# Performance work log

Measured on AMD Instinct MI355X. Metric: run time of the kernel, lower is better.

Reference implementation:

```python
import jax, jax.numpy as jnp
import numpy as np
import math

D_MODEL = 1024
NUM_HEADS = 16
HEAD_DIM = D_MODEL // NUM_HEADS
REPETITIONS = 3
NEG = -10000.0


def setup_inputs() -> dict:
    key = jax.random.key(0)
    ks = jax.random.split(key, 5)
    B, S = 2, 2048
    x = jax.random.normal(ks[0], (B, S, D_MODEL), dtype=jnp.float32)
    Wqkv_w = jax.random.normal(ks[1], (3 * D_MODEL, D_MODEL), dtype=jnp.float32) * (1.0 / math.sqrt(D_MODEL))
    Wqkv_b = jax.random.normal(ks[2], (3 * D_MODEL,), dtype=jnp.float32) * 0.02
    out_w = jax.random.normal(ks[3], (D_MODEL, D_MODEL), dtype=jnp.float32) * (1.0 / math.sqrt(D_MODEL))
    out_b = jax.random.normal(ks[4], (D_MODEL,), dtype=jnp.float32) * 0.02
    return {"x": x, "Wqkv_w": Wqkv_w, "Wqkv_b": Wqkv_b, "out_w": out_w, "out_b": out_b}


def _self_attention(q, k, v, mask):
    # q,k,v: (B,S,H,D); mask: (S,S) additive causal (-10000 above diagonal)
    scale = 1.0 / math.sqrt(q.shape[-1])
    scores = jnp.einsum('bthd,bshd->bhts', q, k * scale) + mask  # (B,H,S,S)
    attn = jax.nn.softmax(scores, axis=-1)
    return jnp.einsum('bhts,bshd->bthd', attn, v)  # (B,S,H,D)


def reference(x, Wqkv_w, Wqkv_b, out_w, out_b):
    B, S, _ = x.shape
    qkv = x @ Wqkv_w.T + Wqkv_b                       # (B,S,3*D_MODEL)
    qkv = qkv.reshape(B, S, 3, NUM_HEADS, HEAD_DIM)
    q, k, v = qkv[:, :, 0], qkv[:, :, 1], qkv[:, :, 2]
    mask = jnp.triu(jnp.full((S, S), NEG, dtype=x.dtype), 1)
    context = _self_attention(q, k, v, mask)
    # recurrent re-attention: rep_dim == 'q' -> query replaced by previous context
    for _ in range(REPETITIONS - 1):
        context = _self_attention(context, k, v, mask)
    out = context.reshape(B, S, D_MODEL) @ out_w.T + out_b
    return out
```

## Files before the change

kernel.cpp:

```cpp
#include <hip/hip_runtime.h>


#define D_MODEL 1024
#define NHEADS  16
#define HD      64
#define SEQ     2048
#define BATCH   2
#define NROWS   (BATCH*SEQ)
#define NQKV    (3*D_MODEL)
#define SCL2F   0.1803368801111601f
#define MASK2   (-14426.950408889634f)

typedef __bf16 bf16x8 __attribute__((ext_vector_type(8)));
typedef float  f32x4  __attribute__((ext_vector_type(4)));
typedef unsigned short us8 __attribute__((ext_vector_type(8)));
typedef unsigned short us4 __attribute__((ext_vector_type(4)));
typedef short  s16x4  __attribute__((ext_vector_type(4)));

__device__ __forceinline__ unsigned short f2bf(float f) {
  unsigned int u = __float_as_uint(f);
  u = (u + 0x7fffu + ((u >> 16) & 1u)) >> 16;
  return (unsigned short)u;
}

union Pack8 { us8 v; unsigned short e[8]; };
union Pack4 { us4 v; unsigned short e[4]; };

__device__ __forceinline__ us8 cvt8(const float4 &a, const float4 &b) {
  Pack8 p;
  p.e[0]=f2bf(a.x); p.e[1]=f2bf(a.y); p.e[2]=f2bf(a.z); p.e[3]=f2bf(a.w);
  p.e[4]=f2bf(b.x); p.e[5]=f2bf(b.y); p.e[6]=f2bf(b.z); p.e[7]=f2bf(b.w);
  return p.v;
}

__device__ __forceinline__ void gl_lds16(const unsigned short* g, unsigned short* l) {
  __builtin_amdgcn_global_load_lds(
      (const __attribute__((address_space(1))) unsigned int*)g,
      (__attribute__((address_space(3))) unsigned int*)l, 16, 0, 0);
}

#define CVT_N1 (NROWS*D_MODEL)
#define CVT_N2 (NQKV*D_MODEL)
#define CVT_N3 (D_MODEL*D_MODEL)

__global__ __launch_bounds__(256) void cvt_all(
    const float* __restrict__ x, const float* __restrict__ wq,
    const float* __restrict__ ow,
    unsigned short* __restrict__ xb, unsigned short* __restrict__ wqb,
    unsigned short* __restrict__ owb)
{
  size_t i = ((size_t)blockIdx.x * 256 + threadIdx.x) * 8;
  const float* src; unsigned short* dst; size_t off;
  if (i < CVT_N1)                { src = x;  dst = xb;  off = i; }
  else if (i < CVT_N1 + CVT_N2)  { src = wq; dst = wqb; off = i - CVT_N1; }
  else                           { src = ow; dst = owb; off = i - CVT_N1 - CVT_N2; }
  float4 a = *(const float4*)(src + off);
  float4 b = *(const float4*)(src + off + 4);
  *(us8*)(dst + off) = cvt8(a, b);
}

__global__ __launch_bounds__(256) void qkv_gemm(
    const unsigned short* __restrict__ xb, const unsigned short* __restrict__ wqb,
    const float* __restrict__ bias,
    unsigned short* __restrict__ q, unsigned short* __restrict__ k,
    unsigned short* __restrict__ vT)
{
  __shared__ __align__(16) unsigned short smem[2*128*64];
  unsigned short* As = smem;
  unsigned short* Bs = smem + 128*64;
  const int tid = threadIdx.x;
  const int m0 = blockIdx.y * 128, n0 = blockIdx.x * 128;
  const int wave = tid >> 6, lane = tid & 63;
  const int wm = (wave >> 1) * 64, wn = (wave & 1) * 64;
  const int lrow = lane & 15, quad = lane >> 4;

  const int dr = lane >> 3;
  const int pg = lane & 7;
  const int sg = (pg ^ dr) * 8;
  const unsigned short* gA[4]; const unsigned short* gB[4];
  unsigned short *lA[4], *lB[4];
  #pragma unroll
  for (int i = 0; i < 4; i++) {
    int c = wave*4 + i;
    gA[i] = xb  + (size_t)(m0 + c*8 + dr) * D_MODEL + sg;
    gB[i] = wqb + (size_t)(n0 + c*8 + dr) * D_MODEL + sg;
    lA[i] = &As[c*512];
    lB[i] = &Bs[c*512];
  }
  const int px0 = (quad ^ (lrow & 7)) * 8;
  const int px1 = ((quad + 4) ^ (lrow & 7)) * 8;

  f32x4 acc[4][4];
  #pragma unroll
  for (int i = 0; i < 4; i++)
    #pragma unroll
    for (int j = 0; j < 4; j++) acc[i][j] = (f32x4){0.f,0.f,0.f,0.f};

  for (int k0 = 0; k0 < D_MODEL; k0 += 64) {
    __syncthreads();
    #pragma unroll
    for (int i = 0; i < 4; i++) { gl_lds16(gA[i] + k0, lA[i]); gl_lds16(gB[i] + k0, lB[i]); }
    __syncthreads();
    bf16x8 af[4][2], bfr[4][2];
    #pragma unroll
    for (int mf = 0; mf < 4; mf++) {
      int row = wm + mf*16 + lrow;
      af[mf][0] = *(const bf16x8*)&As[row*64 + px0];
      af[mf][1] = *(const bf16x8*)&As[row*64 + px1];
    }
    #pragma unroll
    for (int nb = 0; nb < 4; nb++) {
      int row = wn + nb*16 + lrow;
      bfr[nb][0] = *(const bf16x8*)&Bs[row*64 + px0];
      bfr[nb][1] = *(const bf16x8*)&Bs[row*64 + px1];
    }
    #pragma unroll
    for (int h = 0; h < 2; h++)
      #pragma unroll
      for (int mf = 0; mf < 4; mf++)
        #pragma unroll
        for (int nb = 0; nb < 4; nb++)
          acc[mf][nb] = __builtin_amdgcn_mfma_f32_16x16x32_bf16(af[mf][h], bfr[nb][h], acc[mf][nb], 0, 0, 0);
  }

  const int which = n0 >> 10;
  const int b  = m0 >> 11;
  const int s0 = m0 & 2047;
  const int h0 = (n0 & 1023) >> 6;

  __syncthreads();

  if (which < 2) {
    const float scl = (which == 0) ? SCL2F : 1.0f;
    #pragma unroll
    for (int nb = 0; nb < 4; nb++) {
      int n = wn + nb*16 + lrow;
      float bi = bias[n0 + n];
      #pragma unroll
      for (int mf = 0; mf < 4; mf++) {
        int m = wm + mf*16 + quad*4;
        #pragma unroll
        for (int r = 0; r < 4; r++)
          smem[(m + r)*128 + n] = f2bf((acc[mf][nb][r] + bi) * scl);
      }
    }
    __syncthreads();
    unsigned short* dstbase = (which == 0) ? q : k;
    const int hh   = wave >> 1;
    const int half = wave & 1;
    unsigned short* hb = dstbase + ((size_t)((b*NHEADS + h0 + hh)*SEQ + s0))*HD;
    #pragma unroll
    for (int i = 0; i < 8; i++) {
      int off  = half*4096 + i*512 + lane*8;
      int s    = off >> 6;
      int slot = off & 63;
      *(uint4*)(hb + off) = *(const uint4*)&smem[s*128 + hh*64 + slot];
    }
  } else {
    #pragma unroll
    for (int nb = 0; nb < 4; nb++) {
      int n = wn + nb*16 + lrow;
      float bi = bias[n0 + n];
      int sw = (n & 7) << 3;
      #pragma unroll
      for (int mf = 0; mf < 4; mf++) {
        int m = wm + mf*16 + quad*4;
        Pack4 p4;
        #pragma unroll
        for (int r = 0; r < 4; r++) p4.e[r] = f2bf(acc[mf][nb][r] + bi);
        *(us4*)&smem[n*128 + (m ^ sw)] = p4.v;
      }
    }
    __syncthreads();
    #pragma unroll
    for (int i = 0; i < 8; i++) {
      int n  = wave*32 + i*4 + (lane >> 4);
      int mo = (lane & 15) * 8;
      int sw = (n & 7) << 3;
      unsigned short* dst = vT +
          ((size_t)((b*NHEADS + h0 + (n >> 6))*HD + (n & 63)))*SEQ + s0 + mo;
      *(uint4*)dst = *(const uint4*)&smem[n*128 + (mo ^ sw)];
    }
  }
}

#define LDQ 72

__global__ __launch_bounds__(512, 4) void attn3(
    const unsigned short* __restrict__ qg,
    const unsigned short* __restrict__ kg,
    const unsigned short* __restrict__ vTg,
    unsigned short* __restrict__ ctx)
{
  __shared__ __align__(16) unsigned short Ks[4][64*LDQ];
  __shared__ __align__(16) unsigned short Vs[4][64*LDQ];
  unsigned short* QC = &Vs[0][0];

  const int tid  = threadIdx.x;
  const int w    = tid >> 6, lane = tid & 63;
  const int lrow = lane & 15, quad = lane >> 4;
  const int bh = blockIdx.x;
  const int yy = blockIdx.y;
  const int base = (blockIdx.x + yy) & 7;
  const int qt = (yy < 8) ? base : (15 - base);
  const unsigned short* qbase = qg  + (size_t)bh * SEQ * HD;
  const unsigned short* kbase = kg  + (size_t)bh * SEQ * HD;
  const unsigned short* vbase = vTg + (size_t)bh * HD * SEQ;
  unsigned short* cbase = ctx + (size_t)bh * SEQ * HD;

  const int srow = tid >> 3;
  const int sco  = (tid & 7) * 8;
  const int qrow = tid >> 2, qc0 = (tid & 3) * 16;
  const bool vsw = (w & 1);
  const int vq = (quad*4) ^ ((lrow >> 3) << 2);

  {
    const unsigned short* src = qbase + (size_t)(qt*128 + qrow)*HD + qc0;
    *(uint4*)&QC[qrow*LDQ + qc0]     = *(const uint4*)src;
    *(uint4*)&QC[qrow*LDQ + qc0 + 8] = *(const uint4*)(src + 8);
  }
  __syncthreads();

  bf16x8 qb0 = *(const bf16x8*)&QC[(w*16 + lrow)*LDQ + quad*8];
  bf16x8 qb1 = *(const bf16x8*)&QC[(w*16 + lrow)*LDQ + 32 + quad*8];
  __syncthreads();

  const int qwbase = qt*128 + w*16;
  const int npair = qt + 1;

  for (int rep = 0; rep < 3; ++rep) {
    f32x4 od[4];
    #pragma unroll
    for (int df = 0; df < 4; df++) od[df] = (f32x4){0.f,0.f,0.f,0.f};
    float ls = 0.f;

    uint4 ka, kb, va, vb;
    {
      const unsigned short* ks = kbase + (size_t)srow*HD + sco;
      ka = *(const uint4*)ks;  kb = *(const uint4*)(ks + 64*HD);
      const unsigned short* vs = vbase + (size_t)srow*SEQ + sco;
      va = *(const uint4*)vs;  vb = *(const uint4*)(vs + 64);
    }

    for (int t = 0; t < npair; ++t) {
      const int pb = (t & 1) * 2;
      *(uint4*)&Ks[pb][srow*LDQ + sco]   = ka;
      *(uint4*)&Ks[pb+1][srow*LDQ + sco] = kb;
      {
        uint4 vaS = vsw ? make_uint4(va.z, va.w, va.x, va.y) : va;
        uint4 vbS = vsw ? make_uint4(vb.z, vb.w, vb.x, vb.y) : vb;
        *(uint4*)&Vs[pb][srow*LDQ + sco]   = vaS;
        *(uint4*)&Vs[pb+1][srow*LDQ + sco] = vbS;
      }
      if (t + 1 < npair) {
        const unsigned short* ks = kbase + (size_t)((2*t+2)*64 + srow)*HD + sco;
        ka = *(const uint4*)ks;  kb = *(const uint4*)(ks + 64*HD);
        const unsigned short* vs = vbase + (size_t)srow*SEQ + (2*t+2)*64 + sco;
        va = *(const uint4*)vs;  vb = *(const uint4*)(vs + 64);
      }
      __syncthreads();

      #pragma unroll
      for (int half = 0; half < 2; ++half) {
        const int bb = pb + half;
        const int sbase = (2*t + half) * 64;
        if (sbase > qwbase + 15) continue;
        f32x4 sc[4];
        __builtin_amdgcn_s_setprio(1);
        #pragma unroll
        for (int sf = 0; sf < 4; sf++) {
          bf16x8 a0 = *(const bf16x8*)&Ks[bb][(sf*16 + lrow)*LDQ + quad*8];
          bf16x8 a1 = *(const bf16x8*)&Ks[bb][(sf*16 + lrow)*LDQ + 32 + quad*8];
          f32x4 z = (f32x4){0.f,0.f,0.f,0.f};
          z = __builtin_amdgcn_mfma_f32_16x16x32_bf16(a0, qb0, z, 0, 0, 0);
          z = __builtin_amdgcn_mfma_f32_16x16x32_bf16(a1, qb1, z, 0, 0, 0);
          sc[sf] = z;
        }
        __builtin_amdgcn_s_setprio(0);
        if (sbase + 63 > qwbase) {
          int ql = qwbase + lrow;
          #pragma unroll
          for (int sf = 0; sf < 4; sf++)
            #pragma unroll
            for (int r = 0; r < 4; r++)
              if (sbase + sf*16 + quad*4 + r > ql) sc[sf][r] += MASK2;
        }
        s16x4 pf[4];
        float lp = 0.f;
        #pragma unroll
        for (int sf = 0; sf < 4; sf++) {
          Pack4 pk;
          #pragma unroll
          for (int r = 0; r < 4; r++) {
            float pe = __builtin_amdgcn_exp2f(sc[sf][r]);
            lp += pe;
            pk.e[r] = __builtin_bit_cast(unsigned short, (__bf16)pe);
          }
          pf[sf] = __builtin_bit_cast(s16x4, pk.v);
        }
        ls += lp;
        __builtin_amdgcn_s_setprio(1);
        #pragma unroll
        for (int df = 0; df < 4; df++) {
          s16x4 v0 = *(const s16x4*)&Vs[bb][(df*16 + lrow)*LDQ +  0 + vq];
          s16x4 v1 = *(const s16x4*)&Vs[bb][(df*16 + lrow)*LDQ + 16 + vq];
          s16x4 v2 = *(const s16x4*)&Vs[bb][(df*16 + lrow)*LDQ + 32 + vq];
          s16x4 v3 = *(const s16x4*)&Vs[bb][(df*16 + lrow)*LDQ + 48 + vq];
          od[df] = __builtin_amdgcn_mfma_f32_16x16x16bf16_1k(v0, pf[0], od[df], 0, 0, 0);
          od[df] = __builtin_amdgcn_mfma_f32_16x16x16bf16_1k(v1, pf[1], od[df], 0, 0, 0);
          od[df] = __builtin_amdgcn_mfma_f32_16x16x16bf16_1k(v2, pf[2], od[df], 0, 0, 0);
          od[df] = __builtin_amdgcn_mfma_f32_16x16x16bf16_1k(v3, pf[3], od[df], 0, 0, 0);
        }
        __builtin_amdgcn_s_setprio(0);
      }
    }

    ls += __shfl_xor(ls, 16);
    ls += __shfl_xor(ls, 32);

    __syncthreads();
    {
      float f = ((rep < 2) ? SCL2F : 1.0f) / ls;
      #pragma unroll
      for (int df = 0; df < 4; df++) {
        Pack4 pk;
        #pragma unroll
        for (int r = 0; r < 4; r++)
          pk.e[r] = __builtin_bit_cast(unsigned short, (__bf16)(od[df][r] * f));
        *(us4*)&QC[(w*16 + lrow)*LDQ + df*16 + quad*4] = pk.v;
      }
    }
    __syncthreads();
    if (rep < 2) {
      qb0 = *(const bf16x8*)&QC[(w*16 + lrow)*LDQ + quad*8];
      qb1 = *(const bf16x8*)&QC[(w*16 + lrow)*LDQ + 32 + quad*8];
      __syncthreads();
    }
  }

  {
    unsigned short* dst = cbase + (size_t)(qt*128 + qrow)*HD + qc0;
    *(uint4*)dst       = *(const uint4*)&QC[qrow*LDQ + qc0];
    *(uint4*)(dst + 8) = *(const uint4*)&QC[qrow*LDQ + qc0 + 8];
  }
}

__global__ __launch_bounds__(256) void out_gemm(
    const unsigned short* __restrict__ ctx, const unsigned short* __restrict__ owb,
    const float* __restrict__ bias, float* __restrict__ out)
{
  __shared__ __align__(16) unsigned short As[128*64];
  __shared__ __align__(16) unsigned short Bs[64*64];
  const int tid = threadIdx.x;
  const int m0 = blockIdx.y * 128, n0 = blockIdx.x * 64;
  const int wave = tid >> 6, lane = tid & 63;
  const int wm = (wave >> 1) * 64, wn = (wave & 1) * 32;
  const int lrow = lane & 15, quad = lane >> 4;

  const int dr = lane >> 3, pg = lane & 7;
  const int sg = (pg ^ dr) * 8;
  size_t aoff[4]; unsigned short* lA[4];
  #pragma unroll
  for (int i = 0; i < 4; i++) {
    int c = wave*4 + i;
    int row = m0 + c*8 + dr;
    aoff[i] = ((size_t)((row >> 11)*NHEADS)*SEQ + (row & 2047))*HD + sg;
    lA[i] = &As[c*512];
  }
  const unsigned short* gB[2]; unsigned short* lB[2];
  #pragma unroll
  for (int j = 0; j < 2; j++) {
    int c = wave*2 + j;
    gB[j] = owb + (size_t)(n0 + c*8 + dr) * D_MODEL + sg;
    lB[j] = &Bs[c*512];
  }
  const int px0 = (quad ^ (lrow & 7)) * 8;
  const int px1 = ((quad + 4) ^ (lrow & 7)) * 8;

  f32x4 acc[4][2];
  #pragma unroll
  for (int i = 0; i < 4; i++)
    #pragma unroll
    for (int j = 0; j < 2; j++) acc[i][j] = (f32x4){0.f,0.f,0.f,0.f};

  for (int k0 = 0; k0 < D_MODEL; k0 += 64) {
    size_t hoff = (size_t)(k0 >> 6) * SEQ * HD;
    __syncthreads();
    #pragma unroll
    for (int i = 0; i < 4; i++) gl_lds16(ctx + aoff[i] + hoff, lA[i]);
    #pragma unroll
    for (int j = 0; j < 2; j++) gl_lds16(gB[j] + k0, lB[j]);
    __syncthreads();
    bf16x8 af[4][2], bfr[2][2];
    #pragma unroll
    for (int mf = 0; mf < 4; mf++) {
      int row = wm + mf*16 + lrow;
      af[mf][0] = *(const bf16x8*)&As[row*64 + px0];
      af[mf][1] = *(const bf16x8*)&As[row*64 + px1];
    }
    #pragma unroll
    for (int nb = 0; nb < 2; nb++) {
      int row = wn + nb*16 + lrow;
      bfr[nb][0] = *(const bf16x8*)&Bs[row*64 + px0];
      bfr[nb][1] = *(const bf16x8*)&Bs[row*64 + px1];
    }
    #pragma unroll
    for (int h = 0; h < 2; h++)
      #pragma unroll
      for (int mf = 0; mf < 4; mf++)
        #pragma unroll
        for (int nb = 0; nb < 2; nb++)
          acc[mf][nb] = __builtin_amdgcn_mfma_f32_16x16x32_bf16(af[mf][h], bfr[nb][h], acc[mf][nb], 0, 0, 0);
  }

  #pragma unroll
  for (int mf = 0; mf < 4; mf++) {
    #pragma unroll
    for (int nb = 0; nb < 2; nb++) {
      #pragma unroll
      for (int r = 0; r < 4; r++) {
        int mm = m0 + wm + mf*16 + quad*4 + r;
        int n  = n0 + wn + nb*16 + lrow;
        out[(size_t)mm * D_MODEL + n] = acc[mf][nb][r] + bias[n];
      }
    }
  }
}

extern "C" void kernel_launch(void* const* d_in, const int* in_sizes, int n_in,
                              void* d_out, int out_size, void* d_ws, size_t ws_size,
                              hipStream_t stream) {
  (void)in_sizes; (void)n_in; (void)out_size; (void)ws_size;
  const float* x      = (const float*)d_in[0];
  const float* Wqkv_w = (const float*)d_in[1];
  const float* Wqkv_b = (const float*)d_in[2];
  const float* out_w  = (const float*)d_in[3];
  const float* out_b  = (const float*)d_in[4];
  float* out = (float*)d_out;

  unsigned short* ws = (unsigned short*)d_ws;
  unsigned short* xb  = ws;
  unsigned short* wqb = ws + CVT_N1;
  unsigned short* owb = ws + CVT_N1 + CVT_N2;
  unsigned short* q   = ws + CVT_N1 + CVT_N2 + CVT_N3;
  unsigned short* k   = q + (size_t)NROWS*D_MODEL;
  unsigned short* vT  = k + (size_t)NROWS*D_MODEL;
  unsigned short* ctx = xb;

  cvt_all<<<(CVT_N1+CVT_N2+CVT_N3)/(256*8), 256, 0, stream>>>(x, Wqkv_w, out_w, xb, wqb, owb);
  qkv_gemm<<<dim3(NQKV/128, NROWS/128), 256, 0, stream>>>(xb, wqb, Wqkv_b, q, k, vT);
  attn3<<<dim3(BATCH*NHEADS, SEQ/128), 512, 0, stream>>>(q, k, vT, ctx);
  out_gemm<<<dim3(D_MODEL/64, NROWS/128), 256, 0, stream>>>(ctx, owb, out_b, out);
}
```

Measured before the change: 219.2 us.

## Shrink attention query tile to 64 rows with 256-thread blocks

The attention kernel now processes 64 query rows per block with 4 waves instead of 128 rows with 8 waves. The grid doubles to 32 query tiles per head, and each iteration consumes a single 64-key tile instead of a pair. Shared buffers shrink to two stages, and a new four-group tile ordering is meant to balance the causal workload across blocks. This gives more, smaller blocks and less masked-out work per block at the diagonal, but each K/V tile is now reused by fewer queries and there are more barriers per unit of work.

```diff
diff --git a/kernel.cpp b/kernel.cpp
--- a/kernel.cpp
+++ b/kernel.cpp
@@ -186,14 +186,14 @@
 
 #define LDQ 72
 
-__global__ __launch_bounds__(512, 4) void attn3(
+__global__ __launch_bounds__(256, 4) void attn3(
     const unsigned short* __restrict__ qg,
     const unsigned short* __restrict__ kg,
     const unsigned short* __restrict__ vTg,
     unsigned short* __restrict__ ctx)
 {
-  __shared__ __align__(16) unsigned short Ks[4][64*LDQ];
-  __shared__ __align__(16) unsigned short Vs[4][64*LDQ];
+  __shared__ __align__(16) unsigned short Ks[2][64*LDQ];
+  __shared__ __align__(16) unsigned short Vs[2][64*LDQ];
   unsigned short* QC = &Vs[0][0];
 
   const int tid  = threadIdx.x;
@@ -201,23 +201,24 @@
   const int lrow = lane & 15, quad = lane >> 4;
   const int bh = blockIdx.x;
   const int yy = blockIdx.y;
-  const int base = (blockIdx.x + yy) & 7;
-  const int qt = (yy < 8) ? base : (15 - base);
+  const int sgrp = yy >> 3, g = yy & 7;
+  const int e = (bh + g) & 7;
+  const int qt = (sgrp == 0) ? e : (sgrp == 1) ? (31 - e)
+               : (sgrp == 2) ? (15 - e) : (16 + e);
   const unsigned short* qbase = qg  + (size_t)bh * SEQ * HD;
   const unsigned short* kbase = kg  + (size_t)bh * SEQ * HD;
   const unsigned short* vbase = vTg + (size_t)bh * HD * SEQ;
   unsigned short* cbase = ctx + (size_t)bh * SEQ * HD;
 
-  const int srow = tid >> 3;
-  const int sco  = (tid & 7) * 8;
-  const int qrow = tid >> 2, qc0 = (tid & 3) * 16;
-  const bool vsw = (w & 1);
+  const int srow = tid >> 2;
+  const int sco  = (tid & 3) * 16;
+  const bool vsw = (srow >> 3) & 1;
   const int vq = (quad*4) ^ ((lrow >> 3) << 2);
 
   {
-    const unsigned short* src = qbase + (size_t)(qt*128 + qrow)*HD + qc0;
-    *(uint4*)&QC[qrow*LDQ + qc0]     = *(const uint4*)src;
-    *(uint4*)&QC[qrow*LDQ + qc0 + 8] = *(const uint4*)(src + 8);
+    const unsigned short* src = qbase + (size_t)(qt*64 + srow)*HD + sco;
+    *(uint4*)&QC[srow*LDQ + sco]     = *(const uint4*)src;
+    *(uint4*)&QC[srow*LDQ + sco + 8] = *(const uint4*)(src + 8);
   }
   __syncthreads();
 
@@ -225,8 +226,8 @@
   bf16x8 qb1 = *(const bf16x8*)&QC[(w*16 + lrow)*LDQ + 32 + quad*8];
   __syncthreads();
 
-  const int qwbase = qt*128 + w*16;
-  const int npair = qt + 1;
+  const int qwbase = qt*64 + w*16;
+  const int nt = qt + 1;
 
   for (int rep = 0; rep < 3; ++rep) {
     f32x4 od[4];
@@ -234,85 +235,80 @@
     for (int df = 0; df < 4; df++) od[df] = (f32x4){0.f,0.f,0.f,0.f};
     float ls = 0.f;
 
-    uint4 ka, kb, va, vb;
+    uint4 ka0, ka1, va0, va1;
     {
       const unsigned short* ks = kbase + (size_t)srow*HD + sco;
-      ka = *(const uint4*)ks;  kb = *(const uint4*)(ks + 64*HD);
+      ka0 = *(const uint4*)ks;  ka1 = *(const uint4*)(ks + 8);
       const unsigned short* vs = vbase + (size_t)srow*SEQ + sco;
-      va = *(const uint4*)vs;  vb = *(const uint4*)(vs + 64);
-    }
-
-    for (int t = 0; t < npair; ++t) {
-      const int pb = (t & 1) * 2;
-      *(uint4*)&Ks[pb][srow*LDQ + sco]   = ka;
-      *(uint4*)&Ks[pb+1][srow*LDQ + sco] = kb;
+      va0 = *(const uint4*)vs;  va1 = *(const uint4*)(vs + 8);
+    }
+
+    for (int t = 0; t < nt; ++t) {
+      const int bb = t & 1;
+      *(uint4*)&Ks[bb][srow*LDQ + sco]     = ka0;
+      *(uint4*)&Ks[bb][srow*LDQ + sco + 8] = ka1;
       {
-        uint4 vaS = vsw ? make_uint4(va.z, va.w, va.x, va.y) : va;
-        uint4 vbS = vsw ? make_uint4(vb.z, vb.w, vb.x, vb.y) : vb;
-        *(uint4*)&Vs[pb][srow*LDQ + sco]   = vaS;
-        *(uint4*)&Vs[pb+1][srow*LDQ + sco] = vbS;
-      }
-      if (t + 1 < npair) {
-        const unsigned short* ks = kbase + (size_t)((2*t+2)*64 + srow)*HD + sco;
-        ka = *(const uint4*)ks;  kb = *(const uint4*)(ks + 64*HD);
-        const unsigned short* vs = vbase + (size_t)srow*SEQ + (2*t+2)*64 + sco;
-        va = *(const uint4*)vs;  vb = *(const uint4*)(vs + 64);
+        uint4 vaS = vsw ? make_uint4(va0.z, va0.w, va0.x, va0.y) : va0;
+        uint4 vbS = vsw ? make_uint4(va1.z, va1.w, va1.x, va1.y) : va1;
+        *(uint4*)&Vs[bb][srow*LDQ + sco]     = vaS;
+        *(uint4*)&Vs[bb][srow*LDQ + sco + 8] = vbS;
+      }
+      if (t + 1 < nt) {
+        const unsigned short* ks = kbase + (size_t)((t+1)*64 + srow)*HD + sco;
+        ka0 = *(const uint4*)ks;  ka1 = *(const uint4*)(ks + 8);
+        const unsigned short* vs = vbase + (size_t)srow*SEQ + (t+1)*64 + sco;
+        va0 = *(const uint4*)vs;  va1 = *(const uint4*)(vs + 8);
       }
       __syncthreads();
 
-      #pragma unroll
-      for (int half = 0; half < 2; ++half) {
-        const int bb = pb + half;
-        const int sbase = (2*t + half) * 64;
-        if (sbase > qwbase + 15) continue;
-        f32x4 sc[4];
-        __builtin_amdgcn_s_setprio(1);
-        #pragma unroll
-        for (int sf = 0; sf < 4; sf++) {
-          bf16x8 a0 = *(const bf16x8*)&Ks[bb][(sf*16 + lrow)*LDQ + quad*8];
-          bf16x8 a1 = *(const bf16x8*)&Ks[bb][(sf*16 + lrow)*LDQ + 32 + quad*8];
-          f32x4 z = (f32x4){0.f,0.f,0.f,0.f};
-          z = __builtin_amdgcn_mfma_f32_16x16x32_bf16(a0, qb0, z, 0, 0, 0);
-          z = __builtin_amdgcn_mfma_f32_16x16x32_bf16(a1, qb1, z, 0, 0, 0);
-          sc[sf] = z;
+      const int sbase = t * 64;
+      f32x4 sc[4];
+      __builtin_amdgcn_s_setprio(1);
+      #pragma unroll
+      for (int sf = 0; sf < 4; sf++) {
+        bf16x8 a0 = *(const bf16x8*)&Ks[bb][(sf*16 + lrow)*LDQ + quad*8];
+        bf16x8 a1 = *(const bf16x8*)&Ks[bb][(sf*16 + lrow)*LDQ + 32 + quad*8];
+        f32x4 z = (f32x4){0.f,0.f,0.f,0.f};
+        z = __builtin_amdgcn_mfma_f32_16x16x32_bf16(a0, qb0, z, 0, 0, 0);
+        z = __builtin_amdgcn_mfma_f32_16x16x32_bf16(a1, qb1, z, 0, 0, 0);
+        sc[sf] = z;
+      }
+      __builtin_amdgcn_s_setprio(0);
+      if (sbase + 63 > qwbase) {
+        int ql = qwbase + lrow;
+        #pragma unroll
+        for (int sf = 0; sf < 4; sf++)
+          #pragma unroll
+          for (int r = 0; r < 4; r++)
+            if (sbase + sf*16 + quad*4 + r > ql) sc[sf][r] += MASK2;
+      }
+      s16x4 pf[4];
+      float lp = 0.f;
+      #pragma unroll
+      for (int sf = 0; sf < 4; sf++) {
+        Pack4 pk;
+        #pragma unroll
+        for (int r = 0; r < 4; r++) {
+          float pe = __builtin_amdgcn_exp2f(sc[sf][r]);
+          lp += pe;
+          pk.e[r] = __builtin_bit_cast(unsigned short, (__bf16)pe);
         }
-        __builtin_amdgcn_s_setprio(0);
-        if (sbase + 63 > qwbase) {
-          int ql = qwbase + lrow;
-          #pragma unroll
-          for (int sf = 0; sf < 4; sf++)
-            #pragma unroll
-            for (int r = 0; r < 4; r++)
-              if (sbase + sf*16 + quad*4 + r > ql) sc[sf][r] += MASK2;
-        }
-        s16x4 pf[4];
-        float lp = 0.f;
-        #pragma unroll
-        for (int sf = 0; sf < 4; sf++) {
-          Pack4 pk;
-          #pragma unroll
-          for (int r = 0; r < 4; r++) {
-            float pe = __builtin_amdgcn_exp2f(sc[sf][r]);
-            lp += pe;
-            pk.e[r] = __builtin_bit_cast(unsigned short, (__bf16)pe);
-          }
-          pf[sf] = __builtin_bit_cast(s16x4, pk.v);
-        }
-        ls += lp;
-        __builtin_amdgcn_s_setprio(1);
-        #pragma unroll
-        for (int df = 0; df < 4; df++) {
-          s16x4 v0 = *(const s16x4*)&Vs[bb][(df*16 + lrow)*LDQ +  0 + vq];
-          s16x4 v1 = *(const s16x4*)&Vs[bb][(df*16 + lrow)*LDQ + 16 + vq];
-          s16x4 v2 = *(const s16x4*)&Vs[bb][(df*16 + lrow)*LDQ + 32 + vq];
-          s16x4 v3 = *(const s16x4*)&Vs[bb][(df*16 + lrow)*LDQ + 48 + vq];
-          od[df] = __builtin_amdgcn_mfma_f32_16x16x16bf16_1k(v0, pf[0], od[df], 0, 0, 0);
-          od[df] = __builtin_amdgcn_mfma_f32_16x16x16bf16_1k(v1, pf[1], od[df], 0, 0, 0);
-          od[df] = __builtin_amdgcn_mfma_f32_16x16x16bf16_1k(v2, pf[2], od[df], 0, 0, 0);
-          od[df] = __builtin_amdgcn_mfma_f32_16x16x16bf16_1k(v3, pf[3], od[df], 0, 0, 0);
-        }
-        __builtin_amdgcn_s_setprio(0);
-      }
+        pf[sf] = __builtin_bit_cast(s16x4, pk.v);
+      }
+      ls += lp;
+      __builtin_amdgcn_s_setprio(1);
+      #pragma unroll
+      for (int df = 0; df < 4; df++) {
+        s16x4 v0 = *(const s16x4*)&Vs[bb][(df*16 + lrow)*LDQ +  0 + vq];
+        s16x4 v1 = *(const s16x4*)&Vs[bb][(df*16 + lrow)*LDQ + 16 + vq];
+        s16x4 v2 = *(const s16x4*)&Vs[bb][(df*16 + lrow)*LDQ + 32 + vq];
+        s16x4 v3 = *(const s16x4*)&Vs[bb][(df*16 + lrow)*LDQ + 48 + vq];
+        od[df] = __builtin_amdgcn_mfma_f32_16x16x16bf16_1k(v0, pf[0], od[df], 0, 0, 0);
+        od[df] = __builtin_amdgcn_mfma_f32_16x16x16bf16_1k(v1, pf[1], od[df], 0, 0, 0);
+        od[df] = __builtin_amdgcn_mfma_f32_16x16x16bf16_1k(v2, pf[2], od[df], 0, 0, 0);
+        od[df] = __builtin_amdgcn_mfma_f32_16x16x16bf16_1k(v3, pf[3], od[df], 0, 0, 0);
+      }
+      __builtin_amdgcn_s_setprio(0);
     }
 
     ls += __shfl_xor(ls, 16);
@@ -339,9 +335,9 @@
   }
 
   {
-    unsigned short* dst = cbase + (size_t)(qt*128 + qrow)*HD + qc0;
-    *(uint4*)dst       = *(const uint4*)&QC[qrow*LDQ + qc0];
-    *(uint4*)(dst + 8) = *(const uint4*)&QC[qrow*LDQ + qc0 + 8];
+    unsigned short* dst = cbase + (size_t)(qt*64 + srow)*HD + sco;
+    *(uint4*)dst       = *(const uint4*)&QC[srow*LDQ + sco];
+    *(uint4*)(dst + 8) = *(const uint4*)&QC[srow*LDQ + sco + 8];
   }
 }
 
@@ -449,6 +445,6 @@
 
   cvt_all<<<(CVT_N1+CVT_N2+CVT_N3)/(256*8), 256, 0, stream>>>(x, Wqkv_w, out_w, xb, wqb, owb);
   qkv_gemm<<<dim3(NQKV/128, NROWS/128), 256, 0, stream>>>(xb, wqb, Wqkv_b, q, k, vT);
-  attn3<<<dim3(BATCH*NHEADS, SEQ/128), 512, 0, stream>>>(q, k, vT, ctx);
+  attn3<<<dim3(BATCH*NHEADS, 32), 256, 0, stream>>>(q, k, vT, ctx);
   out_gemm<<<dim3(D_MODEL/64, NROWS/128), 256, 0, stream>>>(ctx, owb, out_b, out);
 }
```

Measured after the change: 220.6 us. No clear change (+0.6%).

## Load attention K/V tiles directly into LDS with XOR-swizzled layout

Applied to the files above, without the earlier changes.

Replaces the register-staged K/V prefetch (global load to VGPR, then ds_write) in the attention kernel with direct global-to-LDS loads via gl_lds16, double-buffered across tile pairs. The padded LDQ=72 layout becomes an unpadded 64-wide layout with an XOR swizzle to avoid bank conflicts, and all Q/K/V/context LDS addressing is updated to match. This is meant to cut VGPR pressure and ds_write instructions and reduce LDS footprint. The trade-off is that synchronisation moves to the end of each tile iteration, so correctness depends on the async LDS writes being complete at that barrier.

```diff
diff --git a/kernel.cpp b/kernel.cpp
--- a/kernel.cpp
+++ b/kernel.cpp
@@ -184,16 +184,14 @@
   }
 }
 
-#define LDQ 72
-
 __global__ __launch_bounds__(512, 4) void attn3(
     const unsigned short* __restrict__ qg,
     const unsigned short* __restrict__ kg,
     const unsigned short* __restrict__ vTg,
     unsigned short* __restrict__ ctx)
 {
-  __shared__ __align__(16) unsigned short Ks[4][64*LDQ];
-  __shared__ __align__(16) unsigned short Vs[4][64*LDQ];
+  __shared__ __align__(16) unsigned short Ks[4][64*64];
+  __shared__ __align__(16) unsigned short Vs[4][64*64];
   unsigned short* QC = &Vs[0][0];
 
   const int tid  = threadIdx.x;
@@ -209,20 +207,31 @@
   unsigned short* cbase = ctx + (size_t)bh * SEQ * HD;
 
   const int srow = tid >> 3;
-  const int sco  = (tid & 7) * 8;
-  const int qrow = tid >> 2, qc0 = (tid & 3) * 16;
-  const bool vsw = (w & 1);
-  const int vq = (quad*4) ^ ((lrow >> 3) << 2);
-
+  const int su   = (((tid & 7) ^ (srow & 7)) * 8);
+  unsigned short* const wdst_k[4] = { &Ks[0][(tid>>6)*512], &Ks[1][(tid>>6)*512],
+                                      &Ks[2][(tid>>6)*512], &Ks[3][(tid>>6)*512] };
+  unsigned short* const wdst_v[4] = { &Vs[0][(tid>>6)*512], &Vs[1][(tid>>6)*512],
+                                      &Vs[2][(tid>>6)*512], &Vs[3][(tid>>6)*512] };
+
+  const int kx0 = (quad ^ (lrow & 7)) * 8;
+  const int kx1 = ((quad + 4) ^ (lrow & 7)) * 8;
+  int vx[4];
+  #pragma unroll
+  for (int c = 0; c < 4; c++)
+    vx[c] = (((2*c + (quad >> 1)) ^ (lrow & 7)) * 8) + (quad & 1) * 4;
+
+  const int qrow = tid >> 2, qj = tid & 3;
+  const int qu0 = ((2*qj)     ^ (qrow & 7)) * 8;
+  const int qu1 = ((2*qj + 1) ^ (qrow & 7)) * 8;
   {
-    const unsigned short* src = qbase + (size_t)(qt*128 + qrow)*HD + qc0;
-    *(uint4*)&QC[qrow*LDQ + qc0]     = *(const uint4*)src;
-    *(uint4*)&QC[qrow*LDQ + qc0 + 8] = *(const uint4*)(src + 8);
+    const unsigned short* src = qbase + (size_t)(qt*128 + qrow)*HD + qj*16;
+    *(uint4*)&QC[qrow*64 + qu0] = *(const uint4*)src;
+    *(uint4*)&QC[qrow*64 + qu1] = *(const uint4*)(src + 8);
   }
   __syncthreads();
 
-  bf16x8 qb0 = *(const bf16x8*)&QC[(w*16 + lrow)*LDQ + quad*8];
-  bf16x8 qb1 = *(const bf16x8*)&QC[(w*16 + lrow)*LDQ + 32 + quad*8];
+  bf16x8 qb0 = *(const bf16x8*)&QC[(w*16 + lrow)*64 + kx0];
+  bf16x8 qb1 = *(const bf16x8*)&QC[(w*16 + lrow)*64 + kx1];
   __syncthreads();
 
   const int qwbase = qt*128 + w*16;
@@ -234,31 +243,21 @@
     for (int df = 0; df < 4; df++) od[df] = (f32x4){0.f,0.f,0.f,0.f};
     float ls = 0.f;
 
-    uint4 ka, kb, va, vb;
-    {
-      const unsigned short* ks = kbase + (size_t)srow*HD + sco;
-      ka = *(const uint4*)ks;  kb = *(const uint4*)(ks + 64*HD);
-      const unsigned short* vs = vbase + (size_t)srow*SEQ + sco;
-      va = *(const uint4*)vs;  vb = *(const uint4*)(vs + 64);
-    }
+    gl_lds16(kbase + (size_t)srow*HD + su,        wdst_k[0]);
+    gl_lds16(kbase + (size_t)(64 + srow)*HD + su, wdst_k[1]);
+    gl_lds16(vbase + (size_t)srow*SEQ + su,       wdst_v[0]);
+    gl_lds16(vbase + (size_t)srow*SEQ + 64 + su,  wdst_v[1]);
+    __syncthreads();
 
     for (int t = 0; t < npair; ++t) {
       const int pb = (t & 1) * 2;
-      *(uint4*)&Ks[pb][srow*LDQ + sco]   = ka;
-      *(uint4*)&Ks[pb+1][srow*LDQ + sco] = kb;
-      {
-        uint4 vaS = vsw ? make_uint4(va.z, va.w, va.x, va.y) : va;
-        uint4 vbS = vsw ? make_uint4(vb.z, vb.w, vb.x, vb.y) : vb;
-        *(uint4*)&Vs[pb][srow*LDQ + sco]   = vaS;
-        *(uint4*)&Vs[pb+1][srow*LDQ + sco] = vbS;
-      }
       if (t + 1 < npair) {
-        const unsigned short* ks = kbase + (size_t)((2*t+2)*64 + srow)*HD + sco;
-        ka = *(const uint4*)ks;  kb = *(const uint4*)(ks + 64*HD);
-        const unsigned short* vs = vbase + (size_t)srow*SEQ + (2*t+2)*64 + sco;
-        va = *(const uint4*)vs;  vb = *(const uint4*)(vs + 64);
-      }
-      __syncthreads();
+        const int npb = pb ^ 2;
+        gl_lds16(kbase + (size_t)((2*t+2)*64 + srow)*HD + su, wdst_k[npb]);
+        gl_lds16(kbase + (size_t)((2*t+3)*64 + srow)*HD + su, wdst_k[npb+1]);
+        gl_lds16(vbase + (size_t)srow*SEQ + (2*t+2)*64 + su,  wdst_v[npb]);
+        gl_lds16(vbase + (size_t)srow*SEQ + (2*t+3)*64 + su,  wdst_v[npb+1]);
+      }
 
       #pragma unroll
       for (int half = 0; half < 2; ++half) {
@@ -269,8 +268,8 @@
         __builtin_amdgcn_s_setprio(1);
         #pragma unroll
         for (int sf = 0; sf < 4; sf++) {
-          bf16x8 a0 = *(const bf16x8*)&Ks[bb][(sf*16 + lrow)*LDQ + quad*8];
-          bf16x8 a1 = *(const bf16x8*)&Ks[bb][(sf*16 + lrow)*LDQ + 32 + quad*8];
+          bf16x8 a0 = *(const bf16x8*)&Ks[bb][(sf*16 + lrow)*64 + kx0];
+          bf16x8 a1 = *(const bf16x8*)&Ks[bb][(sf*16 + lrow)*64 + kx1];
           f32x4 z = (f32x4){0.f,0.f,0.f,0.f};
           z = __builtin_amdgcn_mfma_f32_16x16x32_bf16(a0, qb0, z, 0, 0, 0);
           z = __builtin_amdgcn_mfma_f32_16x16x32_bf16(a1, qb1, z, 0, 0, 0);
@@ -302,10 +301,10 @@
         __builtin_amdgcn_s_setprio(1);
         #pragma unroll
         for (int df = 0; df < 4; df++) {
-          s16x4 v0 = *(const s16x4*)&Vs[bb][(df*16 + lrow)*LDQ +  0 + vq];
-          s16x4 v1 = *(const s16x4*)&Vs[bb][(df*16 + lrow)*LDQ + 16 + vq];
-          s16x4 v2 = *(const s16x4*)&Vs[bb][(df*16 + lrow)*LDQ + 32 + vq];
-          s16x4 v3 = *(const s16x4*)&Vs[bb][(df*16 + lrow)*LDQ + 48 + vq];
+          s16x4 v0 = *(const s16x4*)&Vs[bb][(df*16 + lrow)*64 + vx[0]];
+          s16x4 v1 = *(const s16x4*)&Vs[bb][(df*16 + lrow)*64 + vx[1]];
+          s16x4 v2 = *(const s16x4*)&Vs[bb][(df*16 + lrow)*64 + vx[2]];
+          s16x4 v3 = *(const s16x4*)&Vs[bb][(df*16 + lrow)*64 + vx[3]];
           od[df] = __builtin_amdgcn_mfma_f32_16x16x16bf16_1k(v0, pf[0], od[df], 0, 0, 0);
           od[df] = __builtin_amdgcn_mfma_f32_16x16x16bf16_1k(v1, pf[1], od[df], 0, 0, 0);
           od[df] = __builtin_amdgcn_mfma_f32_16x16x16bf16_1k(v2, pf[2], od[df], 0, 0, 0);
@@ -313,12 +312,13 @@
         }
         __builtin_amdgcn_s_setprio(0);
       }
+
+      __syncthreads();
     }
 
     ls += __shfl_xor(ls, 16);
     ls += __shfl_xor(ls, 32);
 
-    __syncthreads();
     {
       float f = ((rep < 2) ? SCL2F : 1.0f) / ls;
       #pragma unroll
@@ -327,21 +327,21 @@
         #pragma unroll
         for (int r = 0; r < 4; r++)
           pk.e[r] = __builtin_bit_cast(unsigned short, (__bf16)(od[df][r] * f));
-        *(us4*)&QC[(w*16 + lrow)*LDQ + df*16 + quad*4] = pk.v;
+        *(us4*)&QC[(w*16 + lrow)*64 + vx[df]] = pk.v;
       }
     }
     __syncthreads();
     if (rep < 2) {
-      qb0 = *(const bf16x8*)&QC[(w*16 + lrow)*LDQ + quad*8];
-      qb1 = *(const bf16x8*)&QC[(w*16 + lrow)*LDQ + 32 + quad*8];
+      qb0 = *(const bf16x8*)&QC[(w*16 + lrow)*64 + kx0];
+      qb1 = *(const bf16x8*)&QC[(w*16 + lrow)*64 + kx1];
       __syncthreads();
     }
   }
 
   {
-    unsigned short* dst = cbase + (size_t)(qt*128 + qrow)*HD + qc0;
-    *(uint4*)dst       = *(const uint4*)&QC[qrow*LDQ + qc0];
-    *(uint4*)(dst + 8) = *(const uint4*)&QC[qrow*LDQ + qc0 + 8];
+    unsigned short* dst = cbase + (size_t)(qt*128 + qrow)*HD + qj*16;
+    *(uint4*)dst       = *(const uint4*)&QC[qrow*64 + qu0];
+    *(uint4*)(dst + 8) = *(const uint4*)&QC[qrow*64 + qu1];
   }
 }
 
```

Result: slower. 232.0 us (+5.8%).
